# Optimization experiments

Measured on AMD Instinct MI355X. Metric: run time of the kernel, lower is better.

Reference implementation:

```python
import jax, jax.numpy as jnp
import numpy as np

B, TQ, TV, D, UNITS = 16, 2048, 2048, 1024, 1024

def setup_inputs() -> dict:
    key = jax.random.key(0)
    k1, k2, k3 = jax.random.split(key, 3)
    query = jax.random.normal(k1, (B, TQ, UNITS), dtype=jnp.float32)
    values = jax.random.normal(k2, (B, TV, D), dtype=jnp.float32)
    # Glorot-ish scale for the Dense kernel
    W_kernel = jax.random.normal(k3, (D, UNITS), dtype=jnp.float32) * (1.0 / np.sqrt(D))
    W_bias = jnp.zeros((UNITS,), dtype=jnp.float32)
    return {"query": query, "values": values, "W_kernel": W_kernel, "W_bias": W_bias}

def reference(query, values, W_kernel, W_bias):
    # keys = Dense(values): [B, Tv, units]
    keys = jnp.einsum('bvd,du->bvu', values, W_kernel) + W_bias
    # score = query @ keys^T: [B, Tq, Tv]
    score = jnp.einsum('bqu,bvu->bqv', query, keys)
    alignment = jax.nn.softmax(score, axis=-1)
    # context = alignment @ values: [B, Tq, d_v]
    context = jnp.einsum('bqv,bvd->bqd', alignment, values)
    return (context, alignment)
```

## Files before the change

### kernel.cpp

```cpp
#include <hip/hip_runtime.h>
#include <hip/hip_bf16.h>


#define B_  16
#define TQ_ 2048
#define TV_ 2048
#define D_  1024
#define U_  1024

typedef __attribute__((ext_vector_type(8))) short bf16x8;
typedef __attribute__((ext_vector_type(4))) float f32x4;

__device__ __forceinline__ short f2bf(float x) {
    union { float f; unsigned u; } v; v.f = x;
    unsigned r = v.u + 0x7fffu + ((v.u >> 16) & 1u);
    return (short)(r >> 16);
}
__device__ __forceinline__ float bf2f(short h) {
    union { unsigned u; float f; } v;
    v.u = ((unsigned)(unsigned short)h) << 16;
    return v.f;
}

__device__ __forceinline__ void gld16(const short* g, short* l) {
    __builtin_amdgcn_global_load_lds(
        (const __attribute__((address_space(1))) void*)g,
        (__attribute__((address_space(3))) void*)l, 16, 0, 0);
}

template<int SPLIT_OUT>
__global__ __launch_bounds__(256, 2) void gemm_nt_planes(
    const short* __restrict__ Ahi, const short* __restrict__ Alo,
    const short* __restrict__ Bhi, const short* __restrict__ Blo,
    float* __restrict__ C, short* __restrict__ Chi, short* __restrict__ Clo,
    int lda, int ldb, int ldc, int K, size_t sA, size_t sB, size_t sC)
{
    __shared__ short sAhi[128 * 32], sAlo[128 * 32], sBhi[128 * 32], sBlo[128 * 32];
    const int tid = threadIdx.x;
    const int lane = tid & 63, wave = tid >> 6;
    const int wm = (wave >> 1) << 6, wn = (wave & 1) << 6;
    const int l15 = lane & 15, l4 = lane >> 4;
    const int lr = lane >> 2, lc = (lane & 3) << 3;
    const size_t row0 = (size_t)blockIdx.y << 7, col0 = (size_t)blockIdx.x << 7;
    const short* Abh = Ahi + (size_t)blockIdx.z * sA + row0 * (size_t)lda;
    const short* Abl = Alo + (size_t)blockIdx.z * sA + row0 * (size_t)lda;
    const short* Bbh = Bhi + (size_t)blockIdx.z * sB + col0 * (size_t)ldb;
    const short* Bbl = Blo + (size_t)blockIdx.z * sB + col0 * (size_t)ldb;

    f32x4 acc[4][4];
    for (int i = 0; i < 4; ++i)
        for (int j = 0; j < 4; ++j)
            acc[i][j] = (f32x4){0.f, 0.f, 0.f, 0.f};

    for (int kt = 0; kt < K; kt += 32) {
        __syncthreads();
        for (int t = 0; t < 2; ++t) {
            const int rbase = (wave << 5) + (t << 4);
            const size_t ga = (size_t)(rbase + lr) * lda + kt + lc;
            const size_t gb = (size_t)(rbase + lr) * ldb + kt + lc;
            const int lb = rbase << 5;
            gld16(Abh + ga, &sAhi[lb]);
            gld16(Abl + ga, &sAlo[lb]);
            gld16(Bbh + gb, &sBhi[lb]);
            gld16(Bbl + gb, &sBlo[lb]);
        }
        __syncthreads();
        const int ko = l4 << 3;
        bf16x8 ah[4], al[4], bh[4], bl[4];
        for (int i = 0; i < 4; ++i) {
            ah[i] = *(const bf16x8*)&sAhi[((wm + (i << 4) + l15) << 5) + ko];
            al[i] = *(const bf16x8*)&sAlo[((wm + (i << 4) + l15) << 5) + ko];
            bh[i] = *(const bf16x8*)&sBhi[((wn + (i << 4) + l15) << 5) + ko];
            bl[i] = *(const bf16x8*)&sBlo[((wn + (i << 4) + l15) << 5) + ko];
        }
        for (int i = 0; i < 4; ++i)
            for (int j = 0; j < 4; ++j) {
                acc[i][j] = __builtin_amdgcn_mfma_f32_16x16x32_bf16(ah[i], bh[j], acc[i][j], 0, 0, 0);
                acc[i][j] = __builtin_amdgcn_mfma_f32_16x16x32_bf16(ah[i], bl[j], acc[i][j], 0, 0, 0);
                acc[i][j] = __builtin_amdgcn_mfma_f32_16x16x32_bf16(al[i], bh[j], acc[i][j], 0, 0, 0);
            }
    }

    if (SPLIT_OUT) {
        for (int i = 0; i < 4; ++i)
            for (int j = 0; j < 4; ++j)
                for (int r = 0; r < 4; ++r) {
                    const float x = acc[i][j][r];
                    const short h = f2bf(x);
                    const short l = f2bf(x - bf2f(h));
                    const size_t idx = (row0 + wm + (i << 4) + (l4 << 2) + r) * (size_t)ldc
                                       + col0 + wn + (j << 4) + l15;
                    Chi[idx] = h;
                    Clo[idx] = l;
                }
    } else {
        float* Cb = C + (size_t)blockIdx.z * sC;
        for (int i = 0; i < 4; ++i)
            for (int j = 0; j < 4; ++j)
                for (int r = 0; r < 4; ++r)
                    Cb[(row0 + wm + (i << 4) + (l4 << 2) + r) * (size_t)ldc
                       + col0 + wn + (j << 4) + l15] = acc[i][j][r];
    }
}

__global__ __launch_bounds__(256, 2) void gemm_ctx(
    const float* __restrict__ A, const short* __restrict__ Bt, float* __restrict__ C,
    int lda, int ldb, int ldc, int K, size_t sA, size_t sB, size_t sC)
{
    __shared__ short sA16[128 * 32], sB16[128 * 32];
    const int tid = threadIdx.x;
    const int lane = tid & 63, wave = tid >> 6;
    const int wm = (wave >> 1) << 6, wn = (wave & 1) << 6;
    const int l15 = lane & 15, l4 = lane >> 4;
    const int lr = lane >> 2, lc = (lane & 3) << 3;
    const size_t row0 = (size_t)blockIdx.y << 7, col0 = (size_t)blockIdx.x << 7;
    const float* Ab = A + (size_t)blockIdx.z * sA + row0 * (size_t)lda;
    const short* Bb = Bt + (size_t)blockIdx.z * sB + col0 * (size_t)ldb;

    f32x4 acc[4][4];
    for (int i = 0; i < 4; ++i)
        for (int j = 0; j < 4; ++j)
            acc[i][j] = (f32x4){0.f, 0.f, 0.f, 0.f};

    for (int kt = 0; kt < K; kt += 32) {
        __syncthreads();
        for (int r = 0; r < 4; ++r) {
            const int flat = (r << 8) + tid;
            const int row = flat >> 3, c = (flat & 7) << 2;
            const float4 va = *(const float4*)(Ab + (size_t)row * lda + kt + c);
            short4 h;
            h.x = f2bf(va.x); h.y = f2bf(va.y); h.z = f2bf(va.z); h.w = f2bf(va.w);
            *(short4*)&sA16[(row << 5) + c] = h;
        }
        for (int t = 0; t < 2; ++t) {
            const int rbase = (wave << 5) + (t << 4);
            gld16(Bb + (size_t)(rbase + lr) * ldb + kt + lc, &sB16[rbase << 5]);
        }
        __syncthreads();
        const int ko = l4 << 3;
        bf16x8 ah[4], bh[4];
        for (int i = 0; i < 4; ++i) {
            ah[i] = *(const bf16x8*)&sA16[((wm + (i << 4) + l15) << 5) + ko];
            bh[i] = *(const bf16x8*)&sB16[((wn + (i << 4) + l15) << 5) + ko];
        }
        for (int i = 0; i < 4; ++i)
            for (int j = 0; j < 4; ++j)
                acc[i][j] = __builtin_amdgcn_mfma_f32_16x16x32_bf16(ah[i], bh[j], acc[i][j], 0, 0, 0);
    }

    float* Cb = C + (size_t)blockIdx.z * sC;
    for (int i = 0; i < 4; ++i)
        for (int j = 0; j < 4; ++j)
            for (int r = 0; r < 4; ++r)
                Cb[(row0 + wm + (i << 4) + (l4 << 2) + r) * (size_t)ldc
                   + col0 + wn + (j << 4) + l15] = acc[i][j][r];
}

__global__ __launch_bounds__(256) void split_f32(
    const float* __restrict__ X, short* __restrict__ hi, short* __restrict__ lo)
{
    const size_t i = ((size_t)blockIdx.x * 256 + threadIdx.x) << 2;
    const float4 v = *(const float4*)(X + i);
    short4 h, l;
    h.x = f2bf(v.x); l.x = f2bf(v.x - bf2f(h.x));
    h.y = f2bf(v.y); l.y = f2bf(v.y - bf2f(h.y));
    h.z = f2bf(v.z); l.z = f2bf(v.z - bf2f(h.z));
    h.w = f2bf(v.w); l.w = f2bf(v.w - bf2f(h.w));
    *(short4*)(hi + i) = h;
    *(short4*)(lo + i) = l;
}

__global__ __launch_bounds__(256) void split_values(
    const float* __restrict__ V, short* __restrict__ Vhi,
    short* __restrict__ Vlo, short* __restrict__ Vt)
{
    __shared__ float tile[32][33];
    const int b = blockIdx.z;
    const int d0 = blockIdx.x << 5, v0 = blockIdx.y << 5;
    const float* Vb = V + (size_t)b * TV_ * D_;
    const size_t pb = (size_t)b * TV_ * D_;
    short* Vtb = Vt + (size_t)b * D_ * TV_;
    const int tx = threadIdx.x, ty = threadIdx.y;
    for (int k = 0; k < 4; ++k) {
        const int v = v0 + ty + (k << 3);
        const float x = Vb[(size_t)v * D_ + d0 + tx];
        tile[ty + (k << 3)][tx] = x;
        const short h = f2bf(x);
        Vhi[pb + (size_t)v * D_ + d0 + tx] = h;
        Vlo[pb + (size_t)v * D_ + d0 + tx] = f2bf(x - bf2f(h));
    }
    __syncthreads();
    for (int k = 0; k < 4; ++k)
        Vtb[(size_t)(d0 + ty + (k << 3)) * TV_ + v0 + tx] = f2bf(tile[tx][ty + (k << 3)]);
}

__global__ __launch_bounds__(256) void softmax_rows(float* __restrict__ S)
{
    float* p = S + (size_t)blockIdx.x * TV_;
    const int t = threadIdx.x;
    const int lane = t & 63, wave = t >> 6;
    float4 a = *(const float4*)(p + (t << 2));
    float4 b = *(const float4*)(p + 1024 + (t << 2));
    float m = fmaxf(fmaxf(fmaxf(a.x, a.y), fmaxf(a.z, a.w)),
                    fmaxf(fmaxf(b.x, b.y), fmaxf(b.z, b.w)));
    for (int off = 32; off; off >>= 1) m = fmaxf(m, __shfl_xor(m, off, 64));
    __shared__ float redm[4], reds[4];
    if (lane == 0) redm[wave] = m;
    __syncthreads();
    m = fmaxf(fmaxf(redm[0], redm[1]), fmaxf(redm[2], redm[3]));
    a.x = __expf(a.x - m); a.y = __expf(a.y - m);
    a.z = __expf(a.z - m); a.w = __expf(a.w - m);
    b.x = __expf(b.x - m); b.y = __expf(b.y - m);
    b.z = __expf(b.z - m); b.w = __expf(b.w - m);
    float s = a.x + a.y + a.z + a.w + b.x + b.y + b.z + b.w;
    for (int off = 32; off; off >>= 1) s += __shfl_xor(s, off, 64);
    if (lane == 0) reds[wave] = s;
    __syncthreads();
    s = reds[0] + reds[1] + reds[2] + reds[3];
    const float inv = 1.0f / s;
    a.x *= inv; a.y *= inv; a.z *= inv; a.w *= inv;
    b.x *= inv; b.y *= inv; b.z *= inv; b.w *= inv;
    *(float4*)(p + (t << 2)) = a;
    *(float4*)(p + 1024 + (t << 2)) = b;
}

extern "C" void kernel_launch(void* const* d_in, const int* in_sizes, int n_in,
                              void* d_out, int out_size, void* d_ws, size_t ws_size,
                              hipStream_t stream)
{
    const float* query  = (const float*)d_in[0];
    const float* values = (const float*)d_in[1];
    const float* Wk     = (const float*)d_in[2];

    const size_t NQ = (size_t)B_ * TQ_ * D_;
    const size_t NV = (size_t)B_ * TV_ * D_;
    const size_t NW = (size_t)D_ * U_;

    float* context = (float*)d_out;
    float* align   = (float*)d_out + NQ;

    short* Phi = (short*)d_out;
    short* Plo = Phi + NQ;
    short* Qhi = (short*)align;
    short* Qlo = Qhi + NQ;
    short* Whi = (short*)d_ws;
    short* Wlo = Whi + NW;
    short* Vhi = Wlo + NW;
    short* Vlo = Vhi + NV;
    short* Vt  = Vlo + NV;

    split_f32<<<NQ / 1024, 256, 0, stream>>>(query, Qhi, Qlo);
    split_f32<<<NW / 1024, 256, 0, stream>>>(Wk, Whi, Wlo);
    split_values<<<dim3(D_ / 32, TV_ / 32, B_), dim3(32, 8), 0, stream>>>(
        values, Vhi, Vlo, Vt);

    gemm_nt_planes<1><<<dim3(D_ / 128, (B_ * TQ_) / 128, 1), 256, 0, stream>>>(
        Qhi, Qlo, Whi, Wlo, nullptr, Phi, Plo, U_, U_, D_, U_, 0, 0, 0);

    gemm_nt_planes<0><<<dim3(TV_ / 128, TQ_ / 128, B_), 256, 0, stream>>>(
        Phi, Plo, Vhi, Vlo, align, nullptr, nullptr, D_, D_, TV_, D_,
        (size_t)TQ_ * D_, (size_t)TV_ * D_, (size_t)TQ_ * TV_);

    softmax_rows<<<B_ * TQ_, 256, 0, stream>>>(align);

    gemm_ctx<<<dim3(D_ / 128, TQ_ / 128, B_), 256, 0, stream>>>(
        align, Vt, context, TV_, TV_, D_, TV_,
        (size_t)TQ_ * TV_, (size_t)D_ * TV_, (size_t)TQ_ * D_);
}
```

Baseline: 1.566 ms.

## Replace GEMM kernels with 256x256 double-buffered swizzled-LDS MFMA kernel

Introduces gemm8, a 512-thread kernel with 256x256 output tiles, double-buffered LDS, an XOR-swizzled layout and interleaved async global-to-LDS loads and MFMA quads under explicit barriers and setprio. The three-plane bf16 split products now run as sequential K-passes over the planes rather than three MFMAs per step. Softmax also writes a bf16 copy of the alignment so the context GEMM can use the same kernel when workspace allows, falling back to the old fp32-A kernel otherwise. The larger tiles and deeper pipelining aim to cut memory traffic and stalls, at the cost of register pressure and an extra bf16 write of the alignment matrix.

```diff
diff --git a/kernel.cpp b/kernel.cpp
--- a/kernel.cpp
+++ b/kernel.cpp
@@ -28,78 +28,159 @@
         (__attribute__((address_space(3))) void*)l, 16, 0, 0);
 }
 
-template<int SPLIT_OUT>
-__global__ __launch_bounds__(256, 2) void gemm_nt_planes(
+#define MFMA_QUAD(MB, NB)                                                       \
+    __builtin_amdgcn_s_setprio(1);                                              \
+    _Pragma("unroll")                                                           \
+    for (int mf = 0; mf < 4; ++mf)                                              \
+        _Pragma("unroll")                                                       \
+        for (int nf = 0; nf < 2; ++nf)                                          \
+            _Pragma("unroll")                                                   \
+            for (int ks = 0; ks < 2; ++ks)                                      \
+                acc[(MB) + mf][(NB) + nf] =                                     \
+                    __builtin_amdgcn_mfma_f32_16x16x32_bf16(                    \
+                        afr[mf][ks], bfr[(NB) + nf][ks],                        \
+                        acc[(MB) + mf][(NB) + nf], 0, 0, 0);                    \
+    __builtin_amdgcn_s_setprio(0);
+
+template<int NPLANES, int SPLIT_OUT, int KT>
+__global__ __launch_bounds__(512, 2) void gemm8(
     const short* __restrict__ Ahi, const short* __restrict__ Alo,
     const short* __restrict__ Bhi, const short* __restrict__ Blo,
     float* __restrict__ C, short* __restrict__ Chi, short* __restrict__ Clo,
-    int lda, int ldb, int ldc, int K, size_t sA, size_t sB, size_t sC)
-{
-    __shared__ short sAhi[128 * 32], sAlo[128 * 32], sBhi[128 * 32], sBlo[128 * 32];
-    const int tid = threadIdx.x;
-    const int lane = tid & 63, wave = tid >> 6;
-    const int wm = (wave >> 1) << 6, wn = (wave & 1) << 6;
-    const int l15 = lane & 15, l4 = lane >> 4;
-    const int lr = lane >> 2, lc = (lane & 3) << 3;
-    const size_t row0 = (size_t)blockIdx.y << 7, col0 = (size_t)blockIdx.x << 7;
-    const short* Abh = Ahi + (size_t)blockIdx.z * sA + row0 * (size_t)lda;
-    const short* Abl = Alo + (size_t)blockIdx.z * sA + row0 * (size_t)lda;
-    const short* Bbh = Bhi + (size_t)blockIdx.z * sB + col0 * (size_t)ldb;
-    const short* Bbl = Blo + (size_t)blockIdx.z * sB + col0 * (size_t)ldb;
-
-    f32x4 acc[4][4];
-    for (int i = 0; i < 4; ++i)
+    int lda, int ldb, int ldc, size_t sAz, size_t sBz, size_t sCz)
+{
+    constexpr int NT = NPLANES * KT;
+    __shared__ short sA[2][16384];
+    __shared__ short sB[2][16384];
+
+    const int tid  = threadIdx.x;
+    const int lane = tid & 63, wid = tid >> 6;
+    const int wm = (wid >> 2) << 7;
+    const int wn = (wid & 3) << 6;
+    const int l15 = lane & 15, l4 = lane >> 4, l7 = lane & 7;
+    const int sr   = tid >> 3;
+    const int colS = ((tid & 7) ^ (sr & 7)) << 3;
+    const int wvB  = wid << 9;
+
+    const size_t z    = blockIdx.z;
+    const size_t row0 = (size_t)blockIdx.y << 8;
+    const size_t col0 = (size_t)blockIdx.x << 8;
+    const short* Abh = Ahi + z * sAz + row0 * (size_t)lda;
+    const short* Abl = (NPLANES == 3) ? Alo + z * sAz + row0 * (size_t)lda : nullptr;
+    const short* Bbh = Bhi + z * sBz + col0 * (size_t)ldb;
+    const short* Bbl = (NPLANES == 3) ? Blo + z * sBz + col0 * (size_t)ldb : nullptr;
+
+    auto aSrc = [&](int t) -> const short* {
+        const int p = t / KT;
+        const short* base = (NPLANES == 3 && p == 2) ? Abl : Abh;
+        return base + ((t - p * KT) << 6);
+    };
+    auto bSrc = [&](int t) -> const short* {
+        const int p = t / KT;
+        const short* base = (NPLANES == 3 && p == 1) ? Bbl : Bbh;
+        return base + ((t - p * KT) << 6);
+    };
+    auto stageA = [&](int t, int h) {
+        const short* g = aSrc(t) + (size_t)((h << 7) + sr) * lda + colS;
+        short* l = &sA[t & 1][(h << 13) + wvB];
+        gld16(g, l);
+        gld16(g + (size_t)(lda << 6), l + 4096);
+    };
+    auto stageB = [&](int t, int h) {
+        const short* g = bSrc(t) + (size_t)((h << 7) + sr) * ldb + colS;
+        short* l = &sB[t & 1][(h << 13) + wvB];
+        gld16(g, l);
+        gld16(g + (size_t)(ldb << 6), l + 4096);
+    };
+
+    f32x4 acc[8][4];
+    #pragma unroll
+    for (int i = 0; i < 8; ++i)
+        #pragma unroll
         for (int j = 0; j < 4; ++j)
             acc[i][j] = (f32x4){0.f, 0.f, 0.f, 0.f};
 
-    for (int kt = 0; kt < K; kt += 32) {
-        __syncthreads();
-        for (int t = 0; t < 2; ++t) {
-            const int rbase = (wave << 5) + (t << 4);
-            const size_t ga = (size_t)(rbase + lr) * lda + kt + lc;
-            const size_t gb = (size_t)(rbase + lr) * ldb + kt + lc;
-            const int lb = rbase << 5;
-            gld16(Abh + ga, &sAhi[lb]);
-            gld16(Abl + ga, &sAlo[lb]);
-            gld16(Bbh + gb, &sBhi[lb]);
-            gld16(Bbl + gb, &sBlo[lb]);
-        }
-        __syncthreads();
-        const int ko = l4 << 3;
-        bf16x8 ah[4], al[4], bh[4], bl[4];
-        for (int i = 0; i < 4; ++i) {
-            ah[i] = *(const bf16x8*)&sAhi[((wm + (i << 4) + l15) << 5) + ko];
-            al[i] = *(const bf16x8*)&sAlo[((wm + (i << 4) + l15) << 5) + ko];
-            bh[i] = *(const bf16x8*)&sBhi[((wn + (i << 4) + l15) << 5) + ko];
-            bl[i] = *(const bf16x8*)&sBlo[((wn + (i << 4) + l15) << 5) + ko];
-        }
-        for (int i = 0; i < 4; ++i)
-            for (int j = 0; j < 4; ++j) {
-                acc[i][j] = __builtin_amdgcn_mfma_f32_16x16x32_bf16(ah[i], bh[j], acc[i][j], 0, 0, 0);
-                acc[i][j] = __builtin_amdgcn_mfma_f32_16x16x32_bf16(ah[i], bl[j], acc[i][j], 0, 0, 0);
-                acc[i][j] = __builtin_amdgcn_mfma_f32_16x16x32_bf16(al[i], bh[j], acc[i][j], 0, 0, 0);
-            }
+    stageB(0, 0); stageB(0, 1); stageA(0, 0); stageA(0, 1);
+    stageB(1, 0); stageB(1, 1); stageA(1, 0);
+    asm volatile("s_waitcnt vmcnt(6)" ::: "memory");
+    __builtin_amdgcn_s_barrier();
+
+    #pragma unroll 1
+    for (int t = 0; t < NT; ++t) {
+        const short* sAb = sA[t & 1];
+        const short* sBb = sB[t & 1];
+        bf16x8 afr[4][2], bfr[4][2];
+
+        #pragma unroll
+        for (int nf = 0; nf < 4; ++nf)
+            #pragma unroll
+            for (int ks = 0; ks < 2; ++ks)
+                bfr[nf][ks] = *(const bf16x8*)&sBb[((wn + (nf << 4) + l15) << 6)
+                                + ((((ks << 2) | l4) ^ l7) << 3)];
+        #pragma unroll
+        for (int mf = 0; mf < 4; ++mf)
+            #pragma unroll
+            for (int ks = 0; ks < 2; ++ks)
+                afr[mf][ks] = *(const bf16x8*)&sAb[((wm + (mf << 4) + l15) << 6)
+                                + ((((ks << 2) | l4) ^ l7) << 3)];
+        if (t + 1 < NT) stageA(t + 1, 1);
+        __builtin_amdgcn_s_barrier();
+        asm volatile("s_waitcnt lgkmcnt(0)" ::: "memory");
+        __builtin_amdgcn_sched_barrier(0);
+        MFMA_QUAD(0, 0)
+        __builtin_amdgcn_s_barrier();
+
+        if (t + 2 < NT) stageB(t + 2, 0);
+        __builtin_amdgcn_s_barrier();
+        MFMA_QUAD(0, 2)
+        __builtin_amdgcn_s_barrier();
+
+        #pragma unroll
+        for (int mf = 0; mf < 4; ++mf)
+            #pragma unroll
+            for (int ks = 0; ks < 2; ++ks)
+                afr[mf][ks] = *(const bf16x8*)&sAb[((wm + 64 + (mf << 4) + l15) << 6)
+                                + ((((ks << 2) | l4) ^ l7) << 3)];
+        if (t + 2 < NT) stageB(t + 2, 1);
+        __builtin_amdgcn_s_barrier();
+        asm volatile("s_waitcnt lgkmcnt(0)" ::: "memory");
+        __builtin_amdgcn_sched_barrier(0);
+        MFMA_QUAD(4, 2)
+        __builtin_amdgcn_s_barrier();
+
+        if (t + 2 < NT) stageA(t + 2, 0);
+        __builtin_amdgcn_s_barrier();
+        MFMA_QUAD(4, 0)
+        if (t < NT - 2)       asm volatile("s_waitcnt vmcnt(6)" ::: "memory");
+        else if (t == NT - 2) asm volatile("s_waitcnt vmcnt(0)" ::: "memory");
+        __builtin_amdgcn_s_barrier();
     }
 
     if (SPLIT_OUT) {
-        for (int i = 0; i < 4; ++i)
-            for (int j = 0; j < 4; ++j)
+        #pragma unroll
+        for (int mf = 0; mf < 8; ++mf)
+            #pragma unroll
+            for (int nf = 0; nf < 4; ++nf)
+                #pragma unroll
                 for (int r = 0; r < 4; ++r) {
-                    const float x = acc[i][j][r];
+                    const float x = acc[mf][nf][r];
                     const short h = f2bf(x);
-                    const short l = f2bf(x - bf2f(h));
-                    const size_t idx = (row0 + wm + (i << 4) + (l4 << 2) + r) * (size_t)ldc
-                                       + col0 + wn + (j << 4) + l15;
+                    const short lo = f2bf(x - bf2f(h));
+                    const size_t idx = (row0 + wm + (mf << 4) + (l4 << 2) + r) * (size_t)ldc
+                                       + col0 + wn + (nf << 4) + l15;
                     Chi[idx] = h;
-                    Clo[idx] = l;
+                    Clo[idx] = lo;
                 }
     } else {
-        float* Cb = C + (size_t)blockIdx.z * sC;
-        for (int i = 0; i < 4; ++i)
-            for (int j = 0; j < 4; ++j)
+        float* Cb = C + z * sCz;
+        #pragma unroll
+        for (int mf = 0; mf < 8; ++mf)
+            #pragma unroll
+            for (int nf = 0; nf < 4; ++nf)
+                #pragma unroll
                 for (int r = 0; r < 4; ++r)
-                    Cb[(row0 + wm + (i << 4) + (l4 << 2) + r) * (size_t)ldc
-                       + col0 + wn + (j << 4) + l15] = acc[i][j][r];
+                    Cb[(row0 + wm + (mf << 4) + (l4 << 2) + r) * (size_t)ldc
+                       + col0 + wn + (nf << 4) + l15] = acc[mf][nf][r];
     }
 }
 
@@ -194,7 +275,8 @@
         Vtb[(size_t)(d0 + ty + (k << 3)) * TV_ + v0 + tx] = f2bf(tile[tx][ty + (k << 3)]);
 }
 
-__global__ __launch_bounds__(256) void softmax_rows(float* __restrict__ S)
+__global__ __launch_bounds__(256) void softmax_rows(
+    float* __restrict__ S, short* __restrict__ A16)
 {
     float* p = S + (size_t)blockIdx.x * TV_;
     const int t = threadIdx.x;
@@ -222,6 +304,14 @@
     b.x *= inv; b.y *= inv; b.z *= inv; b.w *= inv;
     *(float4*)(p + (t << 2)) = a;
     *(float4*)(p + 1024 + (t << 2)) = b;
+    if (A16) {
+        short* q = A16 + (size_t)blockIdx.x * TV_;
+        short4 ha, hb;
+        ha.x = f2bf(a.x); ha.y = f2bf(a.y); ha.z = f2bf(a.z); ha.w = f2bf(a.w);
+        hb.x = f2bf(b.x); hb.y = f2bf(b.y); hb.z = f2bf(b.z); hb.w = f2bf(b.w);
+        *(short4*)(q + (t << 2)) = ha;
+        *(short4*)(q + 1024 + (t << 2)) = hb;
+    }
 }
 
 extern "C" void kernel_launch(void* const* d_in, const int* in_sizes, int n_in,
@@ -235,6 +325,7 @@
     const size_t NQ = (size_t)B_ * TQ_ * D_;
     const size_t NV = (size_t)B_ * TV_ * D_;
     const size_t NW = (size_t)D_ * U_;
+    const size_t NA = (size_t)B_ * TQ_ * TV_;
 
     float* context = (float*)d_out;
     float* align   = (float*)d_out + NQ;
@@ -248,22 +339,29 @@
     short* Vhi = Wlo + NW;
     short* Vlo = Vhi + NV;
     short* Vt  = Vlo + NV;
+    const size_t WS_NEED = (2 * NW + 3 * NV + NA) * sizeof(short);
+    short* A16 = (ws_size >= WS_NEED) ? (Vt + NV) : nullptr;
 
     split_f32<<<NQ / 1024, 256, 0, stream>>>(query, Qhi, Qlo);
     split_f32<<<NW / 1024, 256, 0, stream>>>(Wk, Whi, Wlo);
     split_values<<<dim3(D_ / 32, TV_ / 32, B_), dim3(32, 8), 0, stream>>>(
         values, Vhi, Vlo, Vt);
 
-    gemm_nt_planes<1><<<dim3(D_ / 128, (B_ * TQ_) / 128, 1), 256, 0, stream>>>(
-        Qhi, Qlo, Whi, Wlo, nullptr, Phi, Plo, U_, U_, D_, U_, 0, 0, 0);
-
-    gemm_nt_planes<0><<<dim3(TV_ / 128, TQ_ / 128, B_), 256, 0, stream>>>(
-        Phi, Plo, Vhi, Vlo, align, nullptr, nullptr, D_, D_, TV_, D_,
+    gemm8<3, 1, 16><<<dim3(D_ / 256, (B_ * TQ_) / 256, 1), 512, 0, stream>>>(
+        Qhi, Qlo, Whi, Wlo, nullptr, Phi, Plo, U_, U_, D_, 0, 0, 0);
+
+    gemm8<3, 0, 16><<<dim3(TV_ / 256, TQ_ / 256, B_), 512, 0, stream>>>(
+        Phi, Plo, Vhi, Vlo, align, nullptr, nullptr, D_, D_, TV_,
         (size_t)TQ_ * D_, (size_t)TV_ * D_, (size_t)TQ_ * TV_);
 
-    softmax_rows<<<B_ * TQ_, 256, 0, stream>>>(align);
-
-    gemm_ctx<<<dim3(D_ / 128, TQ_ / 128, B_), 256, 0, stream>>>(
-        align, Vt, context, TV_, TV_, D_, TV_,
-        (size_t)TQ_ * TV_, (size_t)D_ * TV_, (size_t)TQ_ * D_);
-}
+    softmax_rows<<<B_ * TQ_, 256, 0, stream>>>(align, A16);
+
+    if (A16)
+        gemm8<1, 0, 32><<<dim3(D_ / 256, TQ_ / 256, B_), 512, 0, stream>>>(
+            A16, nullptr, Vt, nullptr, context, nullptr, nullptr, TV_, TV_, D_,
+            (size_t)TQ_ * TV_, (size_t)D_ * TV_, (size_t)TQ_ * D_);
+    else
+        gemm_ctx<<<dim3(D_ / 128, TQ_ / 128, B_), 256, 0, stream>>>(
+            align, Vt, context, TV_, TV_, D_, TV_,
+            (size_t)TQ_ * TV_, (size_t)D_ * TV_, (size_t)TQ_ * D_);
+}
```

After: 1.528 ms. -2.4%, faster.
